# Performance work log

Hardware: AMD Instinct MI355X
Metric: run time of the kernel (lower is better)

The kernel has to match this reference:

```python
import jax, jax.numpy as jnp
import numpy as np

H = 512          # hidden_dim
T = 80           # future_length
M = 6            # num_modes
OD = 2           # output_dim
B = 2048         # batch
TEMP = 1.2


def _lin_params(key, out_dim, in_dim, scale=0.02):
    kw, kb = jax.random.split(key)
    W = jax.random.normal(kw, (out_dim, in_dim), jnp.float32) * scale
    b = jax.random.normal(kb, (out_dim,), jnp.float32) * scale
    return W, b


def _per_mode(key, out_dim, in_dim, scale=0.02):
    ks = jax.random.split(key, M)
    Ws, bs = [], []
    for k in ks:
        W, b = _lin_params(k, out_dim, in_dim, scale)
        Ws.append(W); bs.append(b)
    return jnp.stack(Ws), jnp.stack(bs)


def setup_inputs() -> dict:
    key = jax.random.key(0)
    ks = jax.random.split(key, 20)
    inp = {}
    inp['composed_features'] = jax.random.normal(ks[0], (B, H), jnp.float32)
    # mode_decoders: Linear(H,2H) ReLU [Dropout] Linear(2H,H) ReLU [Dropout] Linear(H,H)
    inp['md_W1'], inp['md_b1'] = _per_mode(ks[1], 2 * H, H)
    inp['md_W2'], inp['md_b2'] = _per_mode(ks[2], H, 2 * H)
    inp['md_W3'], inp['md_b3'] = _per_mode(ks[3], H, H)
    # initial_hidden_projections: Linear(H, 2H)
    inp['ih_W'], inp['ih_b'] = _per_mode(ks[4], 2 * H, H)
    # time_projection (shared): Linear(1, H//2) ReLU Linear(H//2, H)
    inp['tp_W1'], inp['tp_b1'] = _lin_params(ks[5], H // 2, 1)
    inp['tp_W2'], inp['tp_b2'] = _lin_params(ks[6], H, H // 2)
    # feedback_projections: Linear(OD, H//2)
    inp['fb_W'], inp['fb_b'] = _per_mode(ks[7], H // 2, OD)
    # LSTM (2 layers, torch gate order i,f,g,o), per mode
    inp['l0_Wih'], inp['l0_bih'] = _per_mode(ks[8], 4 * H, H)
    inp['l0_Whh'], inp['l0_bhh'] = _per_mode(ks[9], 4 * H, H)
    inp['l1_Wih'], inp['l1_bih'] = _per_mode(ks[10], 4 * H, H)
    inp['l1_Whh'], inp['l1_bhh'] = _per_mode(ks[11], 4 * H, H)
    # output_projections: Linear(H,H) ReLU [Dropout] Linear(H,OD)
    inp['op_W1'], inp['op_b1'] = _per_mode(ks[12], H, H)
    inp['op_W2'], inp['op_b2'] = _per_mode(ks[13], OD, H)
    # confidence_head (shared): Linear(H, H//2) ReLU [Dropout] Linear(H//2, M)
    inp['cf_W1'], inp['cf_b1'] = _lin_params(ks[14], H // 2, H)
    inp['cf_W2'], inp['cf_b2'] = _lin_params(ks[15], M, H // 2)
    return inp


def _lstm_cell(x, h, c, Wih, Whh, bih, bhh):
    g = x @ Wih.T + h @ Whh.T + (bih + bhh)
    i, f, gg, o = jnp.split(g, 4, axis=-1)
    c_new = jax.nn.sigmoid(f) * c + jax.nn.sigmoid(i) * jnp.tanh(gg)
    h_new = jax.nn.sigmoid(o) * jnp.tanh(c_new)
    return h_new, c_new


def _forward(composed_features,
             md_W1, md_b1, md_W2, md_b2, md_W3, md_b3,
             ih_W, ih_b, tp_W1, tp_b1, tp_W2, tp_b2,
             fb_W, fb_b,
             l0_Wih, l0_bih, l0_Whh, l0_bhh,
             l1_Wih, l1_bih, l1_Whh, l1_bhh,
             op_W1, op_b1, op_W2, op_b2,
             cf_W1, cf_b1, cf_W2, cf_b2):
    x = composed_features
    bsz = x.shape[0]
    # shared time embeddings for all steps: [T, H]
    t_norm = (jnp.arange(T, dtype=jnp.float32) / (T - 1))[:, None]
    time_embs = jax.nn.relu(t_norm @ tp_W1.T + tp_b1) @ tp_W2.T + tp_b2

    def run_mode(mW1, mb1, mW2, mb2, mW3, mb3, iW, ib, fW, fb,
                 W0i, b0i, W0h, b0h, W1i, b1i, W1h, b1h,
                 oW1, ob1, oW2, ob2):
        # mode decoder (dropout = identity in eval)
        mf = jax.nn.relu(x @ mW1.T + mb1)
        mf = jax.nn.relu(mf @ mW2.T + mb2)
        mf = mf @ mW3.T + mb3                      # [B, H]
        init = x @ iW.T + ib                       # [B, 2H]
        h0 = init[:, :H]; c0 = init[:, H:]
        carry = (h0, c0, h0, c0, jnp.zeros((bsz, OD), x.dtype))
        pad = H - H // 2

        def step(carry, te_t):
            h0, c0, h1, c1, prev = carry
            fb_half = prev @ fW.T + fb             # [B, H//2]
            fb_full = jnp.pad(fb_half, ((0, 0), (0, pad)))
            xin = mf + 0.5 * te_t[None, :] + 0.3 * fb_full
            h0, c0 = _lstm_cell(xin, h0, c0, W0i, W0h, b0i, b0h)
            h1, c1 = _lstm_cell(h0, h1, c1, W1i, W1h, b1i, b1h)
            out = jax.nn.relu(h1 @ oW1.T + ob1) @ oW2.T + ob2  # [B, OD]
            return (h0, c0, h1, c1, out), out

        _, outs = jax.lax.scan(step, carry, time_embs)   # [T, B, OD]
        traj = jnp.transpose(outs, (1, 0, 2))            # [B, T, OD]
        return traj.at[:, 0, :].set(0.0)

    trajs = jax.vmap(run_mode)(md_W1, md_b1, md_W2, md_b2, md_W3, md_b3,
                               ih_W, ih_b, fb_W, fb_b,
                               l0_Wih, l0_bih, l0_Whh, l0_bhh,
                               l1_Wih, l1_bih, l1_Whh, l1_bhh,
                               op_W1, op_b1, op_W2, op_b2)  # [M, B, T, OD]
    trajectories = jnp.transpose(trajs, (1, 0, 2, 3))       # [B, M, T, OD]
    logits = jax.nn.relu(x @ cf_W1.T + cf_b1) @ cf_W2.T + cf_b2  # [B, M]
    confidences = jax.nn.softmax(logits / TEMP, axis=-1)
    return trajectories, confidences, logits


def reference(composed_features,
              md_W1, md_b1, md_W2, md_b2, md_W3, md_b3,
              ih_W, ih_b, tp_W1, tp_b1, tp_W2, tp_b2,
              fb_W, fb_b,
              l0_Wih, l0_bih, l0_Whh, l0_bhh,
              l1_Wih, l1_bih, l1_Whh, l1_bhh,
              op_W1, op_b1, op_W2, op_b2,
              cf_W1, cf_b1, cf_W2, cf_b2):
    return _forward(composed_features,
                    md_W1, md_b1, md_W2, md_b2, md_W3, md_b3,
                    ih_W, ih_b, tp_W1, tp_b1, tp_W2, tp_b2,
                    fb_W, fb_b,
                    l0_Wih, l0_bih, l0_Whh, l0_bhh,
                    l1_Wih, l1_bih, l1_Whh, l1_bhh,
                    op_W1, op_b1, op_W2, op_b2,
                    cf_W1, cf_b1, cf_W2, cf_b2)
```

## Files before the change

### kernel.cpp

```cpp
#include <hip/hip_runtime.h>
#include <cstdint>

typedef __bf16 bf16;
typedef __bf16 bf16x8 __attribute__((ext_vector_type(8)));
typedef float f32x4 __attribute__((ext_vector_type(4)));

#define DI __device__ __forceinline__

#define BATCH 2048
#define HD 512
#define NM 6

DI float sigmoidf_(float x){ return 1.0f / (1.0f + __expf(-x)); }
DI float tanhf_(float x){
  float a = __expf(-2.0f * fabsf(x));
  float t = (1.0f - a) / (1.0f + a);
  return __builtin_copysignf(t, x);
}

DI void gload16(const bf16* g, char* l){
  __builtin_amdgcn_global_load_lds(
    (const __attribute__((address_space(1))) void*)g,
    (__attribute__((address_space(3))) void*)l, 16, 0, 0);
}

__global__ void k_diag(float* out, float wsmb){
  if (threadIdx.x == 0 && blockIdx.x == 0) out[0] = wsmb * 1.0e6f;
}

template<bool GATES, bool DUAL>
__global__ void k_pack(bf16* __restrict__ dst, const float* __restrict__ s1,
                       const float* __restrict__ s2, int K, int NROW, int ksplit)
{
  long idx = (long)blockIdx.x * 256 + threadIdx.x;
  int kper = K >> 3;
  int k0 = (int)(idx % kper) * 8;
  long rest = idx / kper;
  int p = (int)(rest % NROW);
  int mm = (int)(rest / NROW);
  int r;
  if (GATES){
    int nb2 = p >> 7, hi = (p >> 6) & 1, g = (p >> 4) & 3, jl = p & 15;
    r = g * 512 + nb2 * 32 + hi * 16 + jl;
  } else r = p;
  const float* src;
  if (DUAL){
    if (k0 >= ksplit) src = s2 + ((long)mm * NROW + r) * ksplit + (k0 - ksplit);
    else              src = s1 + ((long)mm * NROW + r) * ksplit + k0;
  } else {
    src = s1 + ((long)mm * NROW + r) * K + k0;
  }
  f32x4 v0 = *(const f32x4*)(src);
  f32x4 v1 = *(const f32x4*)(src + 4);
  bf16x8 o;
  #pragma unroll
  for (int k = 0; k < 4; ++k){ o[k] = (bf16)v0[k]; o[4+k] = (bf16)v1[k]; }
  *(bf16x8*)(dst + ((long)mm * NROW + p) * K + k0) = o;
}

__global__ void k_temb(bf16* tembb, const float* tpW1, const float* tpb1,
                       const float* tpW2, const float* tpb2)
{
  int t = blockIdx.x; int tid = threadIdx.x;
  __shared__ float rq[256];
  float tn = (t < 80) ? (float)t / 79.0f : 0.0f;
  rq[tid] = fmaxf(tn * tpW1[tid] + tpb1[tid], 0.0f);
  __syncthreads();
  for (int d = tid; d < 512; d += 256){
    float s = tpb2[d];
    const float* w = tpW2 + d * 256;
    for (int q = 0; q < 256; ++q) s += rq[q] * w[q];
    tembb[t * 512 + d] = (bf16)((t < 80) ? 0.5f * s : 0.0f);
  }
}

__global__ void k_biases(float* bias0p, float* bias1p,
                         const float* l0bih, const float* l0bhh,
                         const float* l1bih, const float* l1bhh,
                         const float* l0Wih, const float* fbb)
{
  int idx = blockIdx.x * 256 + threadIdx.x;
  int m = idx >> 11, p = idx & 2047;
  int nb2 = p >> 7, hi = (p >> 6) & 1, g = (p >> 4) & 3, jl = p & 15;
  int r = g * 512 + nb2 * 32 + hi * 16 + jl;
  bias1p[idx] = l1bih[m * 2048 + r] + l1bhh[m * 2048 + r];
  const float* wrow = l0Wih + ((long)m * 2048 + r) * 512;
  const float* fb = fbb + m * 256;
  float acc = 0.0f;
  for (int q = 0; q < 256; ++q) acc += fb[q] * wrow[q];
  bias0p[idx] = l0bih[m * 2048 + r] + l0bhh[m * 2048 + r] + 0.3f * acc;
}

__global__ void k_feffp(float* feffp, const float* fbW, const float* l0Wih)
{
  int idx = blockIdx.x * 256 + threadIdx.x;
  int p = idx & 2047, o = (idx >> 11) & 1, m = idx >> 12;
  int nb2 = p >> 7, hi = (p >> 6) & 1, g = (p >> 4) & 3, jl = p & 15;
  int r = g * 512 + nb2 * 32 + hi * 16 + jl;
  const float* wrow = l0Wih + ((long)m * 2048 + r) * 512;
  float acc = 0.0f;
  for (int q = 0; q < 256; ++q) acc += fbW[((long)m * 256 + q) * 2 + o] * wrow[q];
  feffp[((long)m * 2 + o) * 2048 + p] = 0.3f * acc;
}

__global__ void k_zero(float* part, float* traj)
{
  int i = blockIdx.x * 256 + threadIdx.x;
  part[i] = 0.0f;
  if (i < 24576){
    int od = i & 1, mm = (i >> 1) % 6, b = i / 12;
    traj[b * 960 + mm * 160 + od] = 0.0f;
  }
}

__global__ void k_logits(const bf16* lt1, const float* cfW2, const float* cfb2,
                         float* conf, float* logitsOut)
{
  int b = blockIdx.x * 256 + threadIdx.x;
  float acc[6];
  #pragma unroll
  for (int mm = 0; mm < 6; ++mm) acc[mm] = cfb2[mm];
  for (int q = 0; q < 256; ++q){
    float xv = (float)lt1[b * 256 + q];
    #pragma unroll
    for (int mm = 0; mm < 6; ++mm) acc[mm] += xv * cfW2[mm * 256 + q];
  }
  float mx = acc[0];
  #pragma unroll
  for (int mm = 1; mm < 6; ++mm) mx = fmaxf(mx, acc[mm]);
  float e[6], s = 0.0f;
  #pragma unroll
  for (int mm = 0; mm < 6; ++mm){ e[mm] = __expf((acc[mm] - mx) * (1.0f / 1.2f)); s += e[mm]; }
  float inv = 1.0f / s;
  #pragma unroll
  for (int mm = 0; mm < 6; ++mm){
    logitsOut[b * 6 + mm] = acc[mm];
    conf[b * 6 + mm] = e[mm] * inv;
  }
}

__global__ void k_red(const float* part, const float* opb2, float* traj)
{
  int i = blockIdx.x * 256 + threadIdx.x;
  int m = i >> 11, b = i & 2047;
  const float* pp = part + (long)i * 8;
  float o0 = pp[0] + pp[2] + pp[4] + pp[6] + opb2[m * 2];
  float o1 = pp[1] + pp[3] + pp[5] + pp[7] + opb2[m * 2 + 1];
  traj[(long)b * 960 + m * 160 + 158] = o0;
  traj[(long)b * 960 + m * 160 + 159] = o1;
}

struct GArgs {
  const bf16* A1; const bf16* A2; const bf16* Bw;
  long a1_ms, a2_ms, b_ms;
  int a_ld, K, ksplit, NBt, MBt, tprev;
  const float* biasf; long bias_ms;
  bf16* out_bf; long out_ms; int out_ld;
  float* out_f; long outf_ms;
  const bf16* baseb; long baseb_ms;
  const float* temb; long temb_ms;
  const float* feff; long feff_ms;
  const float* prevp;
  const float* ob2;
  const float* w2;
  float* part;
  float* cbuf; long c_ms;
  bf16* hout; long h_ms;
  bf16* hout2; float* cbuf2;
};

enum { EP_RELU = 0, EP_BF16 = 1, EP_F32 = 2, EP_INIT = 3, EP_LSTM = 4, EP_OUT = 5 };

template<int EP, bool SPLIT, bool FB>
__global__ __launch_bounds__(256, 2)
void gemm_k(GArgs a)
{
  __shared__ __attribute__((aligned(16))) char smem[33792];
  char* As = smem;
  char* Bs = smem + 16384;
  float* Gf = (float*)smem;

  const int id  = blockIdx.x;
  const int id2 = (id & 7) * ((int)gridDim.x >> 3) + (id >> 3);
  const int per = a.MBt * a.NBt;
  const int m   = id2 / per;
  const int rem = id2 - m * per;
  const int mb  = rem / a.NBt;
  const int nb  = rem - mb * a.NBt;

  const int tid = threadIdx.x;
  const int lane = tid & 63;
  const int wid  = tid >> 6;
  const int wr = wid >> 1, wc = wid & 1;

  const bf16* A1m = a.A1 + (long)m * a.a1_ms;
  const bf16* A2m = SPLIT ? (a.A2 + (long)m * a.a2_ms) : nullptr;
  const bf16* Bm  = a.Bw + (long)m * a.b_ms + (long)nb * 128 * a.K;

  f32x4 acc[4][4];
  #pragma unroll
  for (int i = 0; i < 4; ++i)
    #pragma unroll
    for (int j = 0; j < 4; ++j) acc[i][j] = f32x4{0.f, 0.f, 0.f, 0.f};

  const int rl = lane >> 3;
  const int sg = (lane & 7) ^ rl;
  const bf16* a1B[4]; const bf16* a2B[4]; const bf16* bB[4];
  char* ldA[4]; char* ldB[4];
  #pragma unroll
  for (int c = 0; c < 4; ++c){
    int rt = (wid * 4 + c) * 8 + rl;
    a1B[c] = A1m + (long)(mb * 128 + rt) * a.a_ld + sg * 8;
    if (SPLIT) a2B[c] = A2m + (long)(mb * 128 + rt) * a.a_ld + sg * 8;
    bB[c]  = Bm + (long)rt * a.K + sg * 8;
    ldA[c] = As + (wid * 4 + c) * 1024;
    ldB[c] = Bs + (wid * 4 + c) * 1024;
  }
  auto STAGE = [&](int kb){
    int kcol = kb << 6;
    if (SPLIT && kcol >= a.ksplit){
      int kl = kcol - a.ksplit;
      #pragma unroll
      for (int c = 0; c < 4; ++c){ gload16(a2B[c] + kl, ldA[c]); gload16(bB[c] + kcol, ldB[c]); }
    } else {
      #pragma unroll
      for (int c = 0; c < 4; ++c){ gload16(a1B[c] + kcol, ldA[c]); gload16(bB[c] + kcol, ldB[c]); }
    }
  };

  const int nk = a.K >> 6;
  STAGE(0);
  for (int kb = 0; kb < nk; ++kb){
    __syncthreads();
    bf16x8 af[2][4], bg[2][4];
    #pragma unroll
    for (int ks = 0; ks < 2; ++ks){
      #pragma unroll
      for (int f = 0; f < 4; ++f){
        int rr = wr * 64 + f * 16 + (lane & 15);
        int kB = ks * 64 + ((lane >> 4) << 4);
        af[ks][f] = *(const bf16x8*)(As + rr * 128 + (kB ^ ((rr & 7) << 4)));
        int rb = wc * 64 + f * 16 + (lane & 15);
        bg[ks][f] = *(const bf16x8*)(Bs + rb * 128 + (kB ^ ((rb & 7) << 4)));
      }
    }
    __syncthreads();
    if (kb + 1 < nk) STAGE(kb + 1);
    #pragma unroll
    for (int ks = 0; ks < 2; ++ks)
      #pragma unroll
      for (int i = 0; i < 4; ++i)
        #pragma unroll
        for (int j = 0; j < 4; ++j)
          acc[i][j] = __builtin_amdgcn_mfma_f32_16x16x32_bf16(af[ks][i], bg[ks][j], acc[i][j], 0, 0, 0);
  }

  if constexpr (EP == EP_LSTM){
    const int jl = lane & 15;
    const int qr = lane >> 4;
    const int jh = nb * 32 + wc * 16 + jl;
    const long pbase = (long)nb * 128 + wc * 64 + jl;
    float addv[4], f0v[4], f1v[4];
    #pragma unroll
    for (int g = 0; g < 4; ++g){
      long p = pbase + g * 16;
      if constexpr (FB){
        addv[g] = a.temb[(long)m * a.temb_ms + p];
        f0v[g]  = a.feff[(long)m * a.feff_ms + p];
        f1v[g]  = a.feff[(long)m * a.feff_ms + 2048 + p];
      } else {
        addv[g] = a.biasf[(long)m * a.bias_ms + p];
      }
    }
    const bf16* bb = FB ? (a.baseb + (long)m * a.baseb_ms + pbase) : nullptr;
    float* cb = a.cbuf + (long)m * a.c_ms + jh;
    bf16*  hb = a.hout + (long)m * a.h_ms + jh;
    #pragma unroll
    for (int i = 0; i < 4; ++i){
      #pragma unroll
      for (int q = 0; q < 4; ++q){
        int b = mb * 128 + wr * 64 + i * 16 + qr * 4 + q;
        float pv0 = 0.f, pv1 = 0.f;
        if constexpr (FB){
          if (a.tprev >= 0){
            const float* pp = a.prevp + ((long)m * 2048 + b) * 8;
            pv0 = pp[0] + pp[2] + pp[4] + pp[6] + a.ob2[m * 2];
            pv1 = pp[1] + pp[3] + pp[5] + pp[7] + a.ob2[m * 2 + 1];
          }
          if (nb == 0 && wc == 0 && jl == 0 && a.tprev >= 1){
            a.out_f[(long)b * 960 + m * 160 + a.tprev * 2 + 0] = pv0;
            a.out_f[(long)b * 960 + m * 160 + a.tprev * 2 + 1] = pv1;
          }
        }
        float g4[4];
        #pragma unroll
        for (int g = 0; g < 4; ++g){
          float v = acc[i][g][q] + addv[g];
          if constexpr (FB){
            v += (float)bb[(long)b * 2048 + g * 16];
            v += pv0 * f0v[g] + pv1 * f1v[g];
          }
          g4[g] = v;
        }
        long ro = (long)b * HD;
        float ci = sigmoidf_(g4[0]), cf = sigmoidf_(g4[1]);
        float cg = tanhf_(g4[2]),    co = sigmoidf_(g4[3]);
        float cn = cf * cb[ro] + ci * cg;
        cb[ro] = cn;
        hb[ro] = (bf16)(co * tanhf_(cn));
      }
    }
    return;
  }

  if constexpr (EP == EP_OUT){
    __syncthreads();
    float* ps = (float*)smem;
    int colbase = wc * 64 + (lane & 15);
    float bv[4], w0v[4], w1v[4];
    #pragma unroll
    for (int j = 0; j < 4; ++j){
      int p = nb * 128 + colbase + j * 16;
      bv[j]  = a.biasf[(long)m * a.bias_ms + p];
      w0v[j] = a.w2[(long)m * 1024 + p];
      w1v[j] = a.w2[(long)m * 1024 + 512 + p];
    }
    #pragma unroll
    for (int i = 0; i < 4; ++i)
      #pragma unroll
      for (int q = 0; q < 4; ++q){
        float s0 = 0.f, s1 = 0.f;
        #pragma unroll
        for (int j = 0; j < 4; ++j){
          float v = fmaxf(acc[i][j][q] + bv[j], 0.0f);
          s0 += v * w0v[j]; s1 += v * w1v[j];
        }
        #pragma unroll
        for (int o2 = 1; o2 < 16; o2 <<= 1){ s0 += __shfl_xor(s0, o2); s1 += __shfl_xor(s1, o2); }
        if ((lane & 15) == 0){
          int row = wr * 64 + i * 16 + ((lane >> 4) << 2) + q;
          ps[row * 4 + wc * 2 + 0] = s0;
          ps[row * 4 + wc * 2 + 1] = s1;
        }
      }
    __syncthreads();
    if (tid < 128){
      int b = mb * 128 + tid;
      float o0 = ps[tid * 4 + 0] + ps[tid * 4 + 2];
      float o1 = ps[tid * 4 + 1] + ps[tid * 4 + 3];
      a.part[((long)m * 2048 + b) * 8 + nb * 2 + 0] = o0;
      a.part[((long)m * 2048 + b) * 8 + nb * 2 + 1] = o1;
    }
    return;
  }

  #pragma unroll 1
  for (int ph = 0; ph < 2; ++ph){
    __syncthreads();
    if (wc == ph){
      #pragma unroll
      for (int i = 0; i < 4; ++i)
        #pragma unroll
        for (int j = 0; j < 4; ++j)
          #pragma unroll
          for (int q = 0; q < 4; ++q){
            int rr = wr * 64 + i * 16 + ((lane >> 4) << 2) + q;
            int cc = j * 16 + (lane & 15);
            Gf[rr * 66 + cc] = acc[i][j][q];
          }
    }
    __syncthreads();

    #pragma unroll 1
    for (int it = 0; it < 4; ++it){
      int u = it * 256 + tid;
      int r = u >> 3, cg = u & 7;
      int b = mb * 128 + r;
      int p0 = nb * 128 + ph * 64 + cg * 8;
      float v[8];
      #pragma unroll
      for (int k2 = 0; k2 < 8; ++k2){
        v[k2] = Gf[r * 66 + cg * 8 + k2];
        if (a.biasf) v[k2] += a.biasf[(long)m * a.bias_ms + p0 + k2];
        if constexpr (EP == EP_RELU) v[k2] = fmaxf(v[k2], 0.0f);
      }
      if constexpr (EP == EP_F32){
        float* dst = a.out_f + (long)m * a.outf_ms + (long)b * a.out_ld + p0;
        #pragma unroll
        for (int k2 = 0; k2 < 8; ++k2) dst[k2] = v[k2];
      } else if constexpr (EP == EP_INIT){
        if (p0 < HD){
          bf16x8 ov;
          #pragma unroll
          for (int k2 = 0; k2 < 8; ++k2) ov[k2] = (bf16)v[k2];
          *(bf16x8*)(a.hout  + (long)m * a.h_ms + (long)b * HD + p0) = ov;
          *(bf16x8*)(a.hout2 + (long)m * a.h_ms + (long)b * HD + p0) = ov;
        } else {
          int p1 = p0 - HD;
          float* d1 = a.cbuf  + (long)m * a.c_ms + (long)b * HD + p1;
          float* d2 = a.cbuf2 + (long)m * a.c_ms + (long)b * HD + p1;
          #pragma unroll
          for (int k2 = 0; k2 < 8; ++k2){ d1[k2] = v[k2]; d2[k2] = v[k2]; }
        }
      } else {
        bf16x8 ov;
        #pragma unroll
        for (int k2 = 0; k2 < 8; ++k2) ov[k2] = (bf16)v[k2];
        *(bf16x8*)(a.out_bf + (long)m * a.out_ms + (long)b * a.out_ld + p0) = ov;
      }
    }
  }
}

extern "C" void kernel_launch(void* const* d_in, const int* in_sizes, int n_in,
                              void* d_out, int out_size, void* d_ws, size_t ws_size,
                              hipStream_t stream)
{
  (void)in_sizes; (void)n_in; (void)out_size;
  const float* X     = (const float*)d_in[0];
  const float* mdW1  = (const float*)d_in[1];
  const float* mdb1  = (const float*)d_in[2];
  const float* mdW2  = (const float*)d_in[3];
  const float* mdb2  = (const float*)d_in[4];
  const float* mdW3  = (const float*)d_in[5];
  const float* mdb3  = (const float*)d_in[6];
  const float* ihW   = (const float*)d_in[7];
  const float* ihb   = (const float*)d_in[8];
  const float* tpW1  = (const float*)d_in[9];
  const float* tpb1  = (const float*)d_in[10];
  const float* tpW2  = (const float*)d_in[11];
  const float* tpb2  = (const float*)d_in[12];
  const float* fbW   = (const float*)d_in[13];
  const float* fbb   = (const float*)d_in[14];
  const float* l0Wih = (const float*)d_in[15];
  const float* l0bih = (const float*)d_in[16];
  const float* l0Whh = (const float*)d_in[17];
  const float* l0bhh = (const float*)d_in[18];
  const float* l1Wih = (const float*)d_in[19];
  const float* l1bih = (const float*)d_in[20];
  const float* l1Whh = (const float*)d_in[21];
  const float* l1bhh = (const float*)d_in[22];
  const float* opW1  = (const float*)d_in[23];
  const float* opb1  = (const float*)d_in[24];
  const float* opW2  = (const float*)d_in[25];
  const float* opb2  = (const float*)d_in[26];
  const float* cfW1  = (const float*)d_in[27];
  const float* cfb1  = (const float*)d_in[28];
  const float* cfW2  = (const float*)d_in[29];
  const float* cfb2  = (const float*)d_in[30];
  float* out = (float*)d_out;

  const size_t NEED = 211009536;
  if (ws_size < NEED){
    k_diag<<<1, 64, 0, stream>>>(out, (float)(ws_size >> 20));
    return;
  }
  char* ws = (char*)d_ws;
  const long BH = (long)BATCH * HD;

  bf16*  Wp0     = (bf16*) (ws + 0);
  bf16*  Wp1     = (bf16*) (ws + 12582912);
  bf16*  WpO     = (bf16*) (ws + 37748736);
  bf16*  base0p  = (bf16*) (ws + 40894464);
  float* tembW0p = (float*)(ws + 91226112);
  float* bias1p  = (float*)(ws + 97517568);
  float* Feffp   = (float*)(ws + 97566720);
  char*  REG     =          ws + 97763328;
  bf16*  h0b     = (bf16*) (REG + 0);
  bf16*  h1b     = (bf16*) (REG + 25165824);
  float* c0      = (float*)(REG + 50331648);
  float* c1      = (float*)(REG + 75497472);
  char*  MREG    =          ws + 198426624;

  bf16*  W0ip    = (bf16*) (REG + 0);
  bf16*  mdW1p   = (bf16*) (REG + 12582912);
  bf16*  mdW2p   = (bf16*) (REG + 18874368);
  bf16*  mdW3p   = (bf16*) (REG + 25165824);
  bf16*  tembb   = (bf16*) (REG + 28311552);
  float* bias0p  = (float*)(REG + 28442624);
  bf16*  lt1     = (bf16*) (REG + 28491776);
  bf16*  t1buf   = (bf16*) (REG + 29540352);
  bf16*  t2buf   = (bf16*) (REG + 54706176);
  bf16*  mfbuf   = (bf16*) (REG + 67289088);
  bf16*  xb      = (bf16*) (MREG + 0);
  bf16*  ihWp    = (bf16*) (MREG + 2097152);
  bf16*  cfW1p   = (bf16*) (MREG + 8388608);
  float* part    = (float*)(MREG + 8650752);

  k_pack<false,false><<<dim3(512),  256, 0, stream>>>(xb,    X,     nullptr, 512,  2048, 512);
  k_pack<true ,false><<<dim3(3072), 256, 0, stream>>>(Wp0,   l0Whh, nullptr, 512,  2048, 512);
  k_pack<true ,false><<<dim3(3072), 256, 0, stream>>>(W0ip,  l0Wih, nullptr, 512,  2048, 512);
  k_pack<true ,true ><<<dim3(6144), 256, 0, stream>>>(Wp1,   l1Wih, l1Whh,   1024, 2048, 512);
  k_pack<false,false><<<dim3(768),  256, 0, stream>>>(WpO,   opW1,  nullptr, 512,  512,  512);
  k_pack<false,false><<<dim3(1536), 256, 0, stream>>>(mdW1p, mdW1,  nullptr, 512,  1024, 512);
  k_pack<false,false><<<dim3(1536), 256, 0, stream>>>(mdW2p, mdW2,  nullptr, 1024, 512,  1024);
  k_pack<false,false><<<dim3(768),  256, 0, stream>>>(mdW3p, mdW3,  nullptr, 512,  512,  512);
  k_pack<false,false><<<dim3(1536), 256, 0, stream>>>(ihWp,  ihW,   nullptr, 512,  1024, 512);
  k_pack<false,false><<<dim3(64),   256, 0, stream>>>(cfW1p, cfW1,  nullptr, 512,  256,  512);

  k_temb  <<<dim3(128), 256, 0, stream>>>(tembb, tpW1, tpb1, tpW2, tpb2);
  k_biases<<<dim3(48),  256, 0, stream>>>(bias0p, bias1p, l0bih, l0bhh, l1bih, l1bhh, l0Wih, fbb);
  k_feffp <<<dim3(96),  256, 0, stream>>>(Feffp, fbW, l0Wih);
  k_zero  <<<dim3(384), 256, 0, stream>>>(part, out);

  { GArgs g{}; g.A1 = xb; g.a1_ms = 0; g.a_ld = 512; g.Bw = mdW1p; g.b_ms = (long)1024*512;
    g.K = 512; g.ksplit = 512; g.NBt = 8; g.MBt = 16; g.biasf = mdb1; g.bias_ms = 1024;
    g.out_bf = t1buf; g.out_ms = (long)2048*1024; g.out_ld = 1024;
    gemm_k<EP_RELU,false,false><<<dim3(16*8*6), 256, 0, stream>>>(g); }
  { GArgs g{}; g.A1 = t1buf; g.a1_ms = (long)2048*1024; g.a_ld = 1024; g.Bw = mdW2p; g.b_ms = (long)512*1024;
    g.K = 1024; g.ksplit = 1024; g.NBt = 4; g.MBt = 16; g.biasf = mdb2; g.bias_ms = 512;
    g.out_bf = t2buf; g.out_ms = BH; g.out_ld = 512;
    gemm_k<EP_RELU,false,false><<<dim3(16*4*6), 256, 0, stream>>>(g); }
  { GArgs g{}; g.A1 = t2buf; g.a1_ms = BH; g.a_ld = 512; g.Bw = mdW3p; g.b_ms = (long)512*512;
    g.K = 512; g.ksplit = 512; g.NBt = 4; g.MBt = 16; g.biasf = mdb3; g.bias_ms = 512;
    g.out_bf = mfbuf; g.out_ms = BH; g.out_ld = 512;
    gemm_k<EP_BF16,false,false><<<dim3(16*4*6), 256, 0, stream>>>(g); }
  { GArgs g{}; g.A1 = tembb; g.a1_ms = 0; g.a_ld = 512; g.Bw = W0ip; g.b_ms = (long)2048*512;
    g.K = 512; g.ksplit = 512; g.NBt = 16; g.MBt = 1; g.biasf = nullptr;
    g.out_f = tembW0p; g.outf_ms = (long)128*2048; g.out_ld = 2048;
    gemm_k<EP_F32,false,false><<<dim3(1*16*6), 256, 0, stream>>>(g); }
  { GArgs g{}; g.A1 = mfbuf; g.a1_ms = BH; g.a_ld = 512; g.Bw = W0ip; g.b_ms = (long)2048*512;
    g.K = 512; g.ksplit = 512; g.NBt = 16; g.MBt = 16; g.biasf = bias0p; g.bias_ms = 2048;
    g.out_bf = base0p; g.out_ms = (long)2048*2048; g.out_ld = 2048;
    gemm_k<EP_BF16,false,false><<<dim3(16*16*6), 256, 0, stream>>>(g); }
  { GArgs g{}; g.A1 = xb; g.a1_ms = 0; g.a_ld = 512; g.Bw = cfW1p; g.b_ms = 0;
    g.K = 512; g.ksplit = 512; g.NBt = 2; g.MBt = 16; g.biasf = cfb1; g.bias_ms = 0;
    g.out_bf = lt1; g.out_ms = 0; g.out_ld = 256;
    gemm_k<EP_RELU,false,false><<<dim3(16*2*1), 256, 0, stream>>>(g); }
  k_logits<<<dim3(8), 256, 0, stream>>>(lt1, cfW2, cfb2, out + 1966080, out + 1966080 + 12288);
  { GArgs g{}; g.A1 = xb; g.a1_ms = 0; g.a_ld = 512; g.Bw = ihWp; g.b_ms = (long)1024*512;
    g.K = 512; g.ksplit = 512; g.NBt = 8; g.MBt = 16; g.biasf = ihb; g.bias_ms = 1024;
    g.hout = h0b; g.h_ms = BH; g.hout2 = h1b; g.cbuf = c0; g.c_ms = BH; g.cbuf2 = c1;
    gemm_k<EP_INIT,false,false><<<dim3(16*8*6), 256, 0, stream>>>(g); }

  for (int t = 0; t < 80; ++t){
    int cur = t & 1, nxt = cur ^ 1;
    { GArgs g{}; g.A1 = h0b + (size_t)cur * 6 * BH; g.a1_ms = BH; g.a_ld = 512;
      g.Bw = Wp0; g.b_ms = (long)2048*512; g.K = 512; g.ksplit = 512; g.NBt = 16; g.MBt = 16;
      g.tprev = t - 1;
      g.baseb = base0p; g.baseb_ms = (long)2048*2048;
      g.temb = tembW0p + (long)t * 2048; g.temb_ms = (long)128*2048;
      g.feff = Feffp; g.feff_ms = 4096;
      g.prevp = part; g.ob2 = opb2; g.out_f = out;
      g.cbuf = c0; g.c_ms = BH;
      g.hout = h0b + (size_t)nxt * 6 * BH; g.h_ms = BH;
      gemm_k<EP_LSTM,false,true><<<dim3(16*16*6), 256, 0, stream>>>(g); }
    { GArgs g{}; g.A1 = h0b + (size_t)nxt * 6 * BH; g.A2 = h1b + (size_t)cur * 6 * BH;
      g.a1_ms = BH; g.a2_ms = BH; g.a_ld = 512;
      g.Bw = Wp1; g.b_ms = (long)2048*1024; g.K = 1024; g.ksplit = 512; g.NBt = 16; g.MBt = 16;
      g.biasf = bias1p; g.bias_ms = 2048;
      g.cbuf = c1; g.c_ms = BH;
      g.hout = h1b + (size_t)nxt * 6 * BH; g.h_ms = BH;
      gemm_k<EP_LSTM,true,false><<<dim3(16*16*6), 256, 0, stream>>>(g); }
    { GArgs g{}; g.A1 = h1b + (size_t)nxt * 6 * BH; g.a1_ms = BH; g.a_ld = 512;
      g.Bw = WpO; g.b_ms = (long)512*512; g.K = 512; g.ksplit = 512; g.NBt = 4; g.MBt = 16;
      g.biasf = opb1; g.bias_ms = 512;
      g.w2 = opW2; g.part = part;
      gemm_k<EP_OUT,false,false><<<dim3(16*4*6), 256, 0, stream>>>(g); }
  }
  k_red<<<dim3(48), 256, 0, stream>>>(part, opb2, out);
}
```

Baseline: 11.30 ms.

## Reorder layer-0 base gate buffer for vectorized per-thread loads, raise occupancy bound

A new EP_BASE epilogue writes the precomputed layer-0 base gate contribution in a tile-blocked layout. Each thread's four gate values become contiguous, so the per-step LSTM epilogue reads them with one 8-byte vector load instead of four strided scalar loads. This cuts scattered global traffic in the epilogue of the 80-step recurrent kernel. Separately, launch_bounds minimum blocks per SM goes from 2 to 3, which may raise occupancy but can force register spills.

```diff
diff --git a/kernel.cpp b/kernel.cpp
--- a/kernel.cpp
+++ b/kernel.cpp
@@ -3,6 +3,7 @@
 
 typedef __bf16 bf16;
 typedef __bf16 bf16x8 __attribute__((ext_vector_type(8)));
+typedef __bf16 bf16x4 __attribute__((ext_vector_type(4)));
 typedef float f32x4 __attribute__((ext_vector_type(4)));
 
 #define DI __device__ __forceinline__
@@ -169,10 +170,10 @@
   bf16* hout2; float* cbuf2;
 };
 
-enum { EP_RELU = 0, EP_BF16 = 1, EP_F32 = 2, EP_INIT = 3, EP_LSTM = 4, EP_OUT = 5 };
+enum { EP_RELU = 0, EP_BF16 = 1, EP_F32 = 2, EP_INIT = 3, EP_LSTM = 4, EP_OUT = 5, EP_BASE = 6 };
 
 template<int EP, bool SPLIT, bool FB>
-__global__ __launch_bounds__(256, 2)
+__global__ __launch_bounds__(256, 3)
 void gemm_k(GArgs a)
 {
   __shared__ __attribute__((aligned(16))) char smem[33792];
@@ -272,7 +273,8 @@
         addv[g] = a.biasf[(long)m * a.bias_ms + p];
       }
     }
-    const bf16* bb = FB ? (a.baseb + (long)m * a.baseb_ms + pbase) : nullptr;
+    const bf16* bb = FB ? (a.baseb + (long)m * a.baseb_ms + (long)nb * 2048 * 128
+                           + wc * 64 + jl * 4) : nullptr;
     float* cb = a.cbuf + (long)m * a.c_ms + jh;
     bf16*  hb = a.hout + (long)m * a.h_ms + jh;
     #pragma unroll
@@ -281,7 +283,9 @@
       for (int q = 0; q < 4; ++q){
         int b = mb * 128 + wr * 64 + i * 16 + qr * 4 + q;
         float pv0 = 0.f, pv1 = 0.f;
+        bf16x4 bv4;
         if constexpr (FB){
+          bv4 = *(const bf16x4*)(bb + (long)b * 128);
           if (a.tprev >= 0){
             const float* pp = a.prevp + ((long)m * 2048 + b) * 8;
             pv0 = pp[0] + pp[2] + pp[4] + pp[6] + a.ob2[m * 2];
@@ -297,7 +301,7 @@
         for (int g = 0; g < 4; ++g){
           float v = acc[i][g][q] + addv[g];
           if constexpr (FB){
-            v += (float)bb[(long)b * 2048 + g * 16];
+            v += (float)bv4[g];
             v += pv0 * f0v[g] + pv1 * f1v[g];
           }
           g4[g] = v;
@@ -308,6 +312,28 @@
         float cn = cf * cb[ro] + ci * cg;
         cb[ro] = cn;
         hb[ro] = (bf16)(co * tanhf_(cn));
+      }
+    }
+    return;
+  }
+
+  if constexpr (EP == EP_BASE){
+    const int jl = lane & 15;
+    const int qr = lane >> 4;
+    const long pbase = (long)nb * 128 + wc * 64 + jl;
+    float addv[4];
+    #pragma unroll
+    for (int g = 0; g < 4; ++g) addv[g] = a.biasf[(long)m * a.bias_ms + pbase + g * 16];
+    bf16* dst = a.out_bf + (long)m * a.out_ms + (long)nb * 2048 * 128 + wc * 64 + jl * 4;
+    #pragma unroll
+    for (int i = 0; i < 4; ++i){
+      #pragma unroll
+      for (int q = 0; q < 4; ++q){
+        int b = mb * 128 + wr * 64 + i * 16 + qr * 4 + q;
+        bf16x4 ov;
+        #pragma unroll
+        for (int g = 0; g < 4; ++g) ov[g] = (bf16)(acc[i][g][q] + addv[g]);
+        *(bf16x4*)(dst + (long)b * 128) = ov;
       }
     }
     return;
@@ -461,7 +487,7 @@
   bf16*  Wp0     = (bf16*) (ws + 0);
   bf16*  Wp1     = (bf16*) (ws + 12582912);
   bf16*  WpO     = (bf16*) (ws + 37748736);
-  bf16*  base0p  = (bf16*) (ws + 40894464);
+  bf16*  base0r  = (bf16*) (ws + 40894464);
   float* tembW0p = (float*)(ws + 91226112);
   float* bias1p  = (float*)(ws + 97517568);
   float* Feffp   = (float*)(ws + 97566720);
@@ -521,8 +547,8 @@
     gemm_k<EP_F32,false,false><<<dim3(1*16*6), 256, 0, stream>>>(g); }
   { GArgs g{}; g.A1 = mfbuf; g.a1_ms = BH; g.a_ld = 512; g.Bw = W0ip; g.b_ms = (long)2048*512;
     g.K = 512; g.ksplit = 512; g.NBt = 16; g.MBt = 16; g.biasf = bias0p; g.bias_ms = 2048;
-    g.out_bf = base0p; g.out_ms = (long)2048*2048; g.out_ld = 2048;
-    gemm_k<EP_BF16,false,false><<<dim3(16*16*6), 256, 0, stream>>>(g); }
+    g.out_bf = base0r; g.out_ms = (long)2048*2048;
+    gemm_k<EP_BASE,false,false><<<dim3(16*16*6), 256, 0, stream>>>(g); }
   { GArgs g{}; g.A1 = xb; g.a1_ms = 0; g.a_ld = 512; g.Bw = cfW1p; g.b_ms = 0;
     g.K = 512; g.ksplit = 512; g.NBt = 2; g.MBt = 16; g.biasf = cfb1; g.bias_ms = 0;
     g.out_bf = lt1; g.out_ms = 0; g.out_ld = 256;
@@ -538,7 +564,7 @@
     { GArgs g{}; g.A1 = h0b + (size_t)cur * 6 * BH; g.a1_ms = BH; g.a_ld = 512;
       g.Bw = Wp0; g.b_ms = (long)2048*512; g.K = 512; g.ksplit = 512; g.NBt = 16; g.MBt = 16;
       g.tprev = t - 1;
-      g.baseb = base0p; g.baseb_ms = (long)2048*2048;
+      g.baseb = base0r; g.baseb_ms = (long)2048*2048;
       g.temb = tembW0p + (long)t * 2048; g.temb_ms = (long)128*2048;
       g.feff = Feffp; g.feff_ms = 4096;
       g.prevp = part; g.ob2 = opb2; g.out_f = out;
```

Result: slower. 13.66 ms (+21.0%).
